# Kernel tuning notes

Hardware: AMD Instinct MI355X
Metric: run time of the kernel (lower is better)

## Reference

```python
import jax, jax.numpy as jnp
import numpy as np

N, P, H, C, E = 50000, 128, 64, 2, 1600000


def setup_inputs() -> dict:
    key = jax.random.key(0)
    ks = jax.random.split(key, 8)
    x = jax.random.normal(ks[0], (N, P), dtype=jnp.float32)
    edge_index = jax.random.randint(ks[1], (2, E), 0, N, dtype=jnp.int32)
    # glorot-ish init for linear weights of the three GCNConv layers
    W1 = jax.random.normal(ks[2], (P, H), dtype=jnp.float32) / np.sqrt(P)
    b1 = jnp.zeros((H,), dtype=jnp.float32)
    W2 = jax.random.normal(ks[3], (H, 2 * H), dtype=jnp.float32) / np.sqrt(H)
    b2 = jnp.zeros((2 * H,), dtype=jnp.float32)
    W3 = jax.random.normal(ks[4], (2 * H, C), dtype=jnp.float32) / np.sqrt(2 * H)
    b3 = jnp.zeros((C,), dtype=jnp.float32)
    return {"x": x, "edge_index": edge_index, "W1": W1, "b1": b1,
            "W2": W2, "b2": b2, "W3": W3, "b3": b3}


def reference(x, edge_index, W1, b1, W2, b2, W3, b3):
    n = x.shape[0]
    # PyG gcn_norm: add self-loops, symmetric D^-1/2 A D^-1/2 normalization
    loops = jnp.arange(n, dtype=edge_index.dtype)
    row = jnp.concatenate([edge_index[0], loops])  # source nodes
    col = jnp.concatenate([edge_index[1], loops])  # target nodes
    deg = jax.ops.segment_sum(jnp.ones_like(row, dtype=x.dtype), col, num_segments=n)
    dinv = jnp.where(deg > 0, jax.lax.rsqrt(deg), 0.0)
    norm = dinv[row] * dinv[col]  # per-edge coefficient [E+N]

    def gcn_conv(h, W, b):
        h = h @ W  # linear transform first (PyG GCNConv order)
        out = jax.ops.segment_sum(norm[:, None] * h[row], col, num_segments=n)
        return out + b

    h = jax.nn.relu(gcn_conv(x, W1, b1))
    # dropout is identity in eval mode
    h = jax.nn.relu(gcn_conv(h, W2, b2))
    h = gcn_conv(h, W3, b3)
    return jax.nn.log_softmax(h, axis=1)
```

## Files before the change

### kernel.cpp

```cpp
#include <hip/hip_runtime.h>
#include <hip/hip_fp16.h>

constexpr int P  = 128;
constexpr int H  = 64;
constexpr int H2 = 128;
constexpr int C  = 2;

constexpr int BW_LOG = 7;
constexpr int BWID   = 128;
constexpr int NBMAX  = 512;
constexpr int T1     = 8192;
constexpr int CAP2   = 15360;

__device__ __forceinline__ unsigned packh2(float a, float b){
  unsigned short la = __half_as_ushort(__float2half_rn(a));
  unsigned short lb = __half_as_ushort(__float2half_rn(b));
  return (unsigned)la | ((unsigned)lb << 16);
}

__global__ void k_zero(int* __restrict__ p, int n){
  int i = blockIdx.x*blockDim.x + threadIdx.x;
  if(i<n) p[i]=0;
}

__global__ __launch_bounds__(256) void k_bhist(const int* __restrict__ col,
                                               int* __restrict__ bcnt, int e, int nb){
  __shared__ int h[NBMAX];
  for(int i=threadIdx.x;i<nb;i+=256) h[i]=0;
  __syncthreads();
  int b0 = blockIdx.x*2048;
  #pragma unroll
  for(int u=0;u<8;u++){
    int idx = b0 + u*256 + threadIdx.x;
    if(idx<e) atomicAdd(&h[col[idx]>>BW_LOG], 1);
  }
  __syncthreads();
  for(int i=threadIdx.x;i<nb;i+=256) if(h[i]) atomicAdd(&bcnt[i], h[i]);
}

__global__ __launch_bounds__(NBMAX) void k_bscan(const int* __restrict__ bcnt,
                                                 int* __restrict__ bstart,
                                                 int* __restrict__ bcursor, int nb){
  __shared__ int sm[NBMAX];
  int t = threadIdx.x;
  int v = (t<nb)? bcnt[t] : 0;
  sm[t]=v; __syncthreads();
  for(int d=1; d<NBMAX; d<<=1){
    int u = (t>=d)? sm[t-d] : 0;
    __syncthreads();
    sm[t]+=u;
    __syncthreads();
  }
  if(t<nb){ int s = sm[t]-v; bstart[t]=s; bcursor[t]=s; }
}

__global__ __launch_bounds__(1024) void k_part(const int* __restrict__ row,
                                               const int* __restrict__ col,
                                               int* __restrict__ bcursor,
                                               unsigned* __restrict__ pairs, int e, int nb){
  __shared__ unsigned stage[T1];
  __shared__ int hist[NBMAX];
  __shared__ int base[NBMAX];
  __shared__ int gpos[NBMAX];
  int tid = threadIdx.x;
  int e0 = blockIdx.x*T1;
  int cnt = min(T1, e-e0);
  for(int i=tid;i<nb;i+=1024) hist[i]=0;
  __syncthreads();
  int myb[8]; int myrank[8]; unsigned mypack[8];
  #pragma unroll
  for(int u=0;u<8;u++){
    int idx = u*1024 + tid;
    if(idx<cnt){
      int c = col[e0+idx], r = row[e0+idx];
      int b = c>>BW_LOG;
      myb[u] = b;
      mypack[u] = ((unsigned)r<<BW_LOG) | (unsigned)(c & (BWID-1));
      myrank[u] = atomicAdd(&hist[b], 1);
    } else myb[u] = -1;
  }
  __syncthreads();
  if(tid<NBMAX) base[tid] = (tid<nb)? hist[tid] : 0;
  __syncthreads();
  for(int d=1; d<NBMAX; d<<=1){
    int u2 = 0;
    if(tid<NBMAX && tid>=d) u2 = base[tid-d];
    __syncthreads();
    if(tid<NBMAX) base[tid] += u2;
    __syncthreads();
  }
  if(tid<nb){
    int ex = base[tid] - hist[tid];
    base[tid] = ex;
    gpos[tid] = atomicAdd(&bcursor[tid], hist[tid]);
  }
  __syncthreads();
  #pragma unroll
  for(int u=0;u<8;u++){
    if(myb[u]>=0) stage[ base[myb[u]] + myrank[u] ] = mypack[u];
  }
  __syncthreads();
  int wave = tid>>6, lane = tid&63;
  for(int b=wave; b<nb; b+=16){
    int len = hist[b], lo = base[b], go = gpos[b];
    for(int k=lane; k<len; k+=64) pairs[go+k] = stage[lo+k];
  }
}

__global__ __launch_bounds__(256) void k_csr(const unsigned* __restrict__ pairs,
                                             const int* __restrict__ bstart,
                                             const int* __restrict__ bcnt,
                                             unsigned* __restrict__ srcA,
                                             int* __restrict__ rowptr,
                                             float* __restrict__ dinv,
                                             int n, int e){
  __shared__ int hist[BWID];
  __shared__ int base[BWID];
  __shared__ int cur[BWID];
  __shared__ unsigned stageS[CAP2];
  int b = blockIdx.x, tid = threadIdx.x;
  int lo = bstart[b], cnt = bcnt[b];
  if(tid<BWID) hist[tid]=0;
  __syncthreads();
  for(int i=tid;i<cnt;i+=256) atomicAdd(&hist[pairs[lo+i] & (BWID-1)], 1);
  __syncthreads();
  if(tid<BWID) base[tid] = hist[tid];
  __syncthreads();
  for(int d=1; d<BWID; d<<=1){
    int u = 0;
    if(tid<BWID && tid>=d) u = base[tid-d];
    __syncthreads();
    if(tid<BWID) base[tid] += u;
    __syncthreads();
  }
  if(tid<BWID){
    int ex = base[tid] - hist[tid];
    base[tid] = ex;
    cur[tid] = ex;
    int node = (b<<BW_LOG) + tid;
    if(node<n){
      rowptr[node] = lo + ex;
      dinv[node]   = rsqrtf((float)hist[tid] + 1.0f);
    }
  }
  if(b==0 && tid==0) rowptr[n] = e;
  __syncthreads();
  if(cnt<=CAP2){
    for(int i=tid;i<cnt;i+=256){
      unsigned p = pairs[lo+i];
      int pos = atomicAdd(&cur[p & (BWID-1)], 1);
      stageS[pos] = p & ~0x7Fu;
    }
    __syncthreads();
    for(int i=tid;i<cnt;i+=256) srcA[lo+i] = stageS[i];
  } else {
    for(int i=tid;i<cnt;i+=256){
      unsigned p = pairs[lo+i];
      int pos = atomicAdd(&cur[p & (BWID-1)], 1);
      srcA[lo+pos] = p & ~0x7Fu;
    }
  }
}

__global__ __launch_bounds__(256) void k_gemm1(const float* __restrict__ x,
                                               const float* __restrict__ W,
                                               const float* __restrict__ dinv,
                                               unsigned* __restrict__ out, int n){
  __shared__ float xs[64][68];
  __shared__ float ws[64][64];
  int tid = threadIdx.x;
  int tx = tid & 15, ty = tid >> 4;
  int r0 = blockIdx.x*64;
  float acc[4][4] = {};
  const float4* x4 = (const float4*)x;
  const float4* W4 = (const float4*)W;
  for(int kh=0; kh<2; ++kh){
    __syncthreads();
    #pragma unroll
    for(int it=0; it<4; ++it){
      int idx = tid + 256*it;
      int r = idx >> 4, k4 = idx & 15;
      int gr = r0 + r;
      float4 v = (gr<n) ? x4[(size_t)gr*32 + kh*16 + k4] : make_float4(0.f,0.f,0.f,0.f);
      *(float4*)&xs[r][4*k4] = v;
    }
    #pragma unroll
    for(int it=0; it<4; ++it){
      int idx = tid + 256*it;
      int kk = idx >> 4, c4 = idx & 15;
      *(float4*)&ws[kk][4*c4] = W4[(size_t)(kh*64+kk)*16 + c4];
    }
    __syncthreads();
    #pragma unroll 8
    for(int kk=0; kk<64; ++kk){
      float xv0 = xs[4*ty+0][kk];
      float xv1 = xs[4*ty+1][kk];
      float xv2 = xs[4*ty+2][kk];
      float xv3 = xs[4*ty+3][kk];
      float4 wv = *(const float4*)&ws[kk][4*tx];
      acc[0][0] += xv0*wv.x; acc[0][1] += xv0*wv.y; acc[0][2] += xv0*wv.z; acc[0][3] += xv0*wv.w;
      acc[1][0] += xv1*wv.x; acc[1][1] += xv1*wv.y; acc[1][2] += xv1*wv.z; acc[1][3] += xv1*wv.w;
      acc[2][0] += xv2*wv.x; acc[2][1] += xv2*wv.y; acc[2][2] += xv2*wv.z; acc[2][3] += xv2*wv.w;
      acc[3][0] += xv3*wv.x; acc[3][1] += xv3*wv.y; acc[3][2] += xv3*wv.z; acc[3][3] += xv3*wv.w;
    }
  }
  #pragma unroll
  for(int i=0;i<4;i++){
    int gr = r0 + 4*ty + i;
    if(gr<n){
      float d = dinv[gr];
      uint2 w;
      w.x = packh2(acc[i][0]*d, acc[i][1]*d);
      w.y = packh2(acc[i][2]*d, acc[i][3]*d);
      *(uint2*)&out[(size_t)gr*32 + 2*tx] = w;
    }
  }
}

__global__ __launch_bounds__(256) void k_gemm23(const float* __restrict__ a2,
                                                const float* __restrict__ W2,
                                                const float* __restrict__ b2,
                                                const float* __restrict__ W3,
                                                const float* __restrict__ dinv,
                                                float* __restrict__ u3, int n){
  __shared__ float as[64][68];
  __shared__ float ws[64][128];
  __shared__ float w3s[H2*C];
  __shared__ float b2s[H2];
  int tid = threadIdx.x;
  int tx = tid & 15, ty = tid >> 4;
  int r0 = blockIdx.x*64;
  const float4* a4 = (const float4*)a2;
  const float4* W24 = (const float4*)W2;
  #pragma unroll
  for(int it=0; it<4; ++it){
    int idx = tid + 256*it;
    int r = idx >> 4, k4 = idx & 15;
    int gr = r0 + r;
    float4 v = (gr<n) ? a4[(size_t)gr*16 + k4] : make_float4(0.f,0.f,0.f,0.f);
    *(float4*)&as[r][4*k4] = v;
  }
  #pragma unroll
  for(int it=0; it<8; ++it){
    int idx = tid + 256*it;
    int kk = idx >> 5, c4 = idx & 31;
    *(float4*)&ws[kk][4*c4] = W24[(size_t)kk*32 + c4];
  }
  if(tid < H2*C) w3s[tid] = W3[tid];
  if(tid < H2)   b2s[tid] = b2[tid];
  __syncthreads();
  float acc[4][8] = {};
  #pragma unroll 4
  for(int kk=0; kk<64; ++kk){
    float xv0 = as[4*ty+0][kk];
    float xv1 = as[4*ty+1][kk];
    float xv2 = as[4*ty+2][kk];
    float xv3 = as[4*ty+3][kk];
    float4 wa = *(const float4*)&ws[kk][8*tx];
    float4 wb = *(const float4*)&ws[kk][8*tx+4];
    acc[0][0]+=xv0*wa.x; acc[0][1]+=xv0*wa.y; acc[0][2]+=xv0*wa.z; acc[0][3]+=xv0*wa.w;
    acc[0][4]+=xv0*wb.x; acc[0][5]+=xv0*wb.y; acc[0][6]+=xv0*wb.z; acc[0][7]+=xv0*wb.w;
    acc[1][0]+=xv1*wa.x; acc[1][1]+=xv1*wa.y; acc[1][2]+=xv1*wa.z; acc[1][3]+=xv1*wa.w;
    acc[1][4]+=xv1*wb.x; acc[1][5]+=xv1*wb.y; acc[1][6]+=xv1*wb.z; acc[1][7]+=xv1*wb.w;
    acc[2][0]+=xv2*wa.x; acc[2][1]+=xv2*wa.y; acc[2][2]+=xv2*wa.z; acc[2][3]+=xv2*wa.w;
    acc[2][4]+=xv2*wb.x; acc[2][5]+=xv2*wb.y; acc[2][6]+=xv2*wb.z; acc[2][7]+=xv2*wb.w;
    acc[3][0]+=xv3*wa.x; acc[3][1]+=xv3*wa.y; acc[3][2]+=xv3*wa.z; acc[3][3]+=xv3*wa.w;
    acc[3][4]+=xv3*wb.x; acc[3][5]+=xv3*wb.y; acc[3][6]+=xv3*wb.z; acc[3][7]+=xv3*wb.w;
  }
  float p[4][2] = {};
  #pragma unroll
  for(int j=0;j<8;j++){
    int c = 8*tx + j;
    float w30 = w3s[2*c], w31 = w3s[2*c+1], bb = b2s[c];
    #pragma unroll
    for(int i=0;i<4;i++){
      float g = fmaxf(acc[i][j] + bb, 0.f);
      p[i][0] += g*w30;
      p[i][1] += g*w31;
    }
  }
  #pragma unroll
  for(int d=1; d<16; d<<=1){
    #pragma unroll
    for(int i=0;i<4;i++){
      p[i][0] += __shfl_xor(p[i][0], d);
      p[i][1] += __shfl_xor(p[i][1], d);
    }
  }
  if(tx==0){
    #pragma unroll
    for(int i=0;i<4;i++){
      int gr = r0 + 4*ty + i;
      if(gr<n){
        float d = dinv[gr];
        u3[2*gr]   = d*p[i][0];
        u3[2*gr+1] = d*p[i][1];
      }
    }
  }
}

template<int MODE>
__global__ __launch_bounds__(256) void k_pullh(const unsigned* __restrict__ src,
                                               const int* __restrict__ rowptr,
                                               const char* __restrict__ tb0,
                                               const float* __restrict__ dinv,
                                               const float* __restrict__ bias,
                                               void* __restrict__ outp, int n){
  int node = blockIdx.x*4 + (threadIdx.x>>6);
  if(node>=n) return;
  int lane = threadIdx.x & 63;
  int slot = lane >> 3;
  int q    = lane & 7;
  const char* tb = tb0 + q*16;
  __half2 h0 = __float2half2_rn(0.f), h1 = h0, h2v = h0, h3 = h0;
  __half2 g0 = h0, g1 = h0, g2v = h0, g3 = h0;
  int beg = rowptr[node], end = rowptr[node+1];
  int j = beg;
  for(; j+16<=end; j+=16){
    unsigned s0 = src[j+slot], s1 = src[j+8+slot];
    uint4 r0 = *(const uint4*)(tb + s0);
    uint4 r1 = *(const uint4*)(tb + s1);
    const __half2* p0 = (const __half2*)&r0;
    const __half2* p1 = (const __half2*)&r1;
    h0 = __hadd2(h0, p0[0]); h1 = __hadd2(h1, p0[1]);
    h2v= __hadd2(h2v,p0[2]); h3 = __hadd2(h3, p0[3]);
    g0 = __hadd2(g0, p1[0]); g1 = __hadd2(g1, p1[1]);
    g2v= __hadd2(g2v,p1[2]); g3 = __hadd2(g3, p1[3]);
  }
  for(; j+8<=end; j+=8){
    unsigned s = src[j+slot];
    uint4 r = *(const uint4*)(tb + s);
    const __half2* p = (const __half2*)&r;
    h0 = __hadd2(h0, p[0]); h1 = __hadd2(h1, p[1]);
    h2v= __hadd2(h2v,p[2]); h3 = __hadd2(h3, p[3]);
  }
  if(j+slot < end){
    unsigned s = src[j+slot];
    uint4 r = *(const uint4*)(tb + s);
    const __half2* p = (const __half2*)&r;
    g0 = __hadd2(g0, p[0]); g1 = __hadd2(g1, p[1]);
    g2v= __hadd2(g2v,p[2]); g3 = __hadd2(g3, p[3]);
  }
  float a[8];
  {
    float2 fa, fb;
    fa = __half22float2(h0); fb = __half22float2(g0); a[0]=fa.x+fb.x; a[1]=fa.y+fb.y;
    fa = __half22float2(h1); fb = __half22float2(g1); a[2]=fa.x+fb.x; a[3]=fa.y+fb.y;
    fa = __half22float2(h2v);fb = __half22float2(g2v);a[4]=fa.x+fb.x; a[5]=fa.y+fb.y;
    fa = __half22float2(h3); fb = __half22float2(g3); a[6]=fa.x+fb.x; a[7]=fa.y+fb.y;
  }
  #pragma unroll
  for(int d=8; d<64; d<<=1){
    #pragma unroll
    for(int i=0;i<8;i++) a[i] += __shfl_xor(a[i], d);
  }
  if(slot==0){
    uint4 sr = *(const uint4*)(tb + (unsigned)node*128u);
    const __half2* p = (const __half2*)&sr;
    float2 f0 = __half22float2(p[0]), f1 = __half22float2(p[1]);
    float2 f2 = __half22float2(p[2]), f3 = __half22float2(p[3]);
    a[0]+=f0.x; a[1]+=f0.y; a[2]+=f1.x; a[3]+=f1.y;
    a[4]+=f2.x; a[5]+=f2.y; a[6]+=f3.x; a[7]+=f3.y;
    float dv = dinv[node];
    if(MODE==1){
      const float* bq = bias + 8*q;
      float o[8];
      #pragma unroll
      for(int i=0;i<8;i++) o[i] = dv * fmaxf(dv*a[i] + bq[i], 0.f);
      uint4 w;
      w.x = packh2(o[0],o[1]); w.y = packh2(o[2],o[3]);
      w.z = packh2(o[4],o[5]); w.w = packh2(o[6],o[7]);
      ((uint4*)outp)[(size_t)node*8 + q] = w;
    } else {
      float* orow = (float*)outp + (size_t)node*64 + 8*q;
      *(float4*)orow     = make_float4(dv*a[0], dv*a[1], dv*a[2], dv*a[3]);
      *(float4*)(orow+4) = make_float4(dv*a[4], dv*a[5], dv*a[6], dv*a[7]);
    }
  }
}

__global__ __launch_bounds__(256) void k_pull2_lsm(const unsigned* __restrict__ src,
                                                   const int* __restrict__ rowptr,
                                                   const float* __restrict__ u3,
                                                   const float* __restrict__ dinv,
                                                   const float* __restrict__ b3,
                                                   float* __restrict__ out, int n){
  int node = blockIdx.x*16 + (threadIdx.x>>4);
  int l16  = threadIdx.x & 15;
  if(node>=n) return;
  const char* ub = (const char*)u3;
  int beg = rowptr[node], end = rowptr[node+1];
  float p0=0.f, p1=0.f, q0=0.f, q1=0.f;
  int j = beg + l16;
  for(; j+16 < end; j += 32){
    float2 A = *(const float2*)(ub + (src[j]    >> 4));
    float2 B = *(const float2*)(ub + (src[j+16] >> 4));
    p0 += A.x; p1 += A.y; q0 += B.x; q1 += B.y;
  }
  if(j < end){
    float2 A = *(const float2*)(ub + (src[j] >> 4));
    p0 += A.x; p1 += A.y;
  }
  p0 += q0; p1 += q1;
  #pragma unroll
  for(int d=1; d<16; d<<=1){ p0 += __shfl_xor(p0,d); p1 += __shfl_xor(p1,d); }
  if(l16==0){
    float d = dinv[node];
    const float2 self = *(const float2*)(ub + (size_t)node*8);
    float z0 = d*(p0 + self.x) + b3[0];
    float z1 = d*(p1 + self.y) + b3[1];
    float m = fmaxf(z0,z1);
    float l = m + logf(expf(z0-m)+expf(z1-m));
    out[2*node]   = z0-l;
    out[2*node+1] = z1-l;
  }
}

extern "C" void kernel_launch(void* const* d_in, const int* in_sizes, int n_in,
                              void* d_out, int out_size, void* d_ws, size_t ws_size,
                              hipStream_t stream){
  const float* x  = (const float*)d_in[0];
  const int*   ei = (const int*)  d_in[1];
  const float* W1 = (const float*)d_in[2];
  const float* b1 = (const float*)d_in[3];
  const float* W2 = (const float*)d_in[4];
  const float* b2 = (const float*)d_in[5];
  const float* W3 = (const float*)d_in[6];
  const float* b3 = (const float*)d_in[7];
  float* out = (float*)d_out;

  const int n = in_sizes[0] / P;
  const int e = in_sizes[1] / 2;
  const int* row = ei;
  const int* col = ei + e;
  const int nb = (n + BWID - 1) >> BW_LOG;

  float* ws   = (float*)d_ws;
  size_t off = 0;
  float* dinv = ws + off; off += n;
  float* R1   = ws + off; off += (size_t)64*n;
  float* R2   = ws + off; off += (size_t)128*n;
  int* rowptr = (int*)(ws + off); off += n+1;
  unsigned* srcA = (unsigned*)(ws + off); off += e;
  int* bcnt   = (int*)(ws + off); off += NBMAX;
  int* bstart = (int*)(ws + off); off += NBMAX;
  int* bcursor= (int*)(ws + off); off += NBMAX;

  unsigned* pairs = (unsigned*)R2;

  unsigned* u1h = (unsigned*)R1;
  unsigned* g1h = (unsigned*)R2;
  float*    a2  = R2 + (size_t)32*n;
  float*    u3  = R1;

  const int BT = 256;

  k_zero <<<(nb+BT-1)/BT, BT, 0, stream>>>(bcnt, nb);
  k_bhist<<<(e+2047)/2048, BT, 0, stream>>>(col, bcnt, e, nb);
  k_bscan<<<1, NBMAX, 0, stream>>>(bcnt, bstart, bcursor, nb);
  k_part <<<(e+T1-1)/T1, 1024, 0, stream>>>(row, col, bcursor, pairs, e, nb);
  k_csr  <<<nb, BT, 0, stream>>>(pairs, bstart, bcnt, srcA, rowptr, dinv, n, e);

  k_gemm1<<<(n+63)/64, BT, 0, stream>>>(x, W1, dinv, u1h, n);

  const int pg = (n+3)/4;
  k_pullh<1><<<pg, BT, 0, stream>>>(srcA, rowptr, (const char*)u1h, dinv, b1, (void*)g1h, n);
  k_pullh<2><<<pg, BT, 0, stream>>>(srcA, rowptr, (const char*)g1h, dinv, nullptr, (void*)a2, n);

  k_gemm23<<<(n+63)/64, BT, 0, stream>>>(a2, W2, b2, W3, dinv, u3, n);
  k_pull2_lsm<<<(n+15)/16, BT, 0, stream>>>(srcA, rowptr, u3, dinv, b3, out, n);
}
```

Before: 180.3 us.

## Store layer-2 aggregate in fp16, use wave-shuffle scans, unroll gather loop

The second aggregation pass now writes fp16 instead of fp32, and the fused layer-2/3 GEMM reads and converts it. This halves that intermediate's write and read traffic at some precision cost. The block-level shared-memory prefix scans in the partition and CSR kernels are replaced by single-wave register and shuffle scans, which cuts many barriers. The half-precision gather loop gains a 32-edge unrolled stage for more loads in flight, and the zeroing kernel becomes a memset. Buffers are rearranged so u3 sits after the fp16 a2 in R1.

Measured after the change: 179.1 us. Within noise of the previous version (-0.6%).

```diff
diff --git a/kernel.cpp b/kernel.cpp
--- a/kernel.cpp
+++ b/kernel.cpp
@@ -16,11 +16,6 @@
   unsigned short la = __half_as_ushort(__float2half_rn(a));
   unsigned short lb = __half_as_ushort(__float2half_rn(b));
   return (unsigned)la | ((unsigned)lb << 16);
-}
-
-__global__ void k_zero(int* __restrict__ p, int n){
-  int i = blockIdx.x*blockDim.x + threadIdx.x;
-  if(i<n) p[i]=0;
 }
 
 __global__ __launch_bounds__(256) void k_bhist(const int* __restrict__ col,
@@ -65,7 +60,7 @@
   int tid = threadIdx.x;
   int e0 = blockIdx.x*T1;
   int cnt = min(T1, e-e0);
-  for(int i=tid;i<nb;i+=1024) hist[i]=0;
+  for(int i=tid;i<NBMAX;i+=1024) hist[i]=0;
   __syncthreads();
   int myb[8]; int myrank[8]; unsigned mypack[8];
   #pragma unroll
@@ -80,20 +75,21 @@
     } else myb[u] = -1;
   }
   __syncthreads();
-  if(tid<NBMAX) base[tid] = (tid<nb)? hist[tid] : 0;
-  __syncthreads();
-  for(int d=1; d<NBMAX; d<<=1){
-    int u2 = 0;
-    if(tid<NBMAX && tid>=d) u2 = base[tid-d];
-    __syncthreads();
-    if(tid<NBMAX) base[tid] += u2;
-    __syncthreads();
-  }
-  if(tid<nb){
-    int ex = base[tid] - hist[tid];
-    base[tid] = ex;
-    gpos[tid] = atomicAdd(&bcursor[tid], hist[tid]);
-  }
+  if(tid<64){
+    int v[8]; int sum=0;
+    #pragma unroll
+    for(int i=0;i<8;i++) v[i]=hist[tid*8+i];
+    #pragma unroll
+    for(int i=0;i<8;i++){ int t=v[i]; v[i]=sum; sum+=t; }
+    int run=sum;
+    #pragma unroll
+    for(int d=1; d<64; d<<=1){ int u=__shfl_up(run,d); if(tid>=d) run+=u; }
+    int excl = run - sum;
+    #pragma unroll
+    for(int i=0;i<8;i++) base[tid*8+i] = excl + v[i];
+  }
+  __syncthreads();
+  if(tid<nb) gpos[tid] = atomicAdd(&bcursor[tid], hist[tid]);
   __syncthreads();
   #pragma unroll
   for(int u=0;u<8;u++){
@@ -124,18 +120,19 @@
   __syncthreads();
   for(int i=tid;i<cnt;i+=256) atomicAdd(&hist[pairs[lo+i] & (BWID-1)], 1);
   __syncthreads();
-  if(tid<BWID) base[tid] = hist[tid];
-  __syncthreads();
-  for(int d=1; d<BWID; d<<=1){
-    int u = 0;
-    if(tid<BWID && tid>=d) u = base[tid-d];
-    __syncthreads();
-    if(tid<BWID) base[tid] += u;
-    __syncthreads();
-  }
+  if(tid<64){
+    int v0=hist[2*tid], v1=hist[2*tid+1];
+    int sum=v0+v1;
+    int run=sum;
+    #pragma unroll
+    for(int d=1; d<64; d<<=1){ int u=__shfl_up(run,d); if(tid>=d) run+=u; }
+    int excl = run - sum;
+    base[2*tid]   = excl;
+    base[2*tid+1] = excl + v0;
+  }
+  __syncthreads();
   if(tid<BWID){
-    int ex = base[tid] - hist[tid];
-    base[tid] = ex;
+    int ex = base[tid];
     cur[tid] = ex;
     int node = (b<<BW_LOG) + tid;
     if(node<n){
@@ -217,7 +214,7 @@
   }
 }
 
-__global__ __launch_bounds__(256) void k_gemm23(const float* __restrict__ a2,
+__global__ __launch_bounds__(256) void k_gemm23(const unsigned* __restrict__ a2h,
                                                 const float* __restrict__ W2,
                                                 const float* __restrict__ b2,
                                                 const float* __restrict__ W3,
@@ -230,15 +227,20 @@
   int tid = threadIdx.x;
   int tx = tid & 15, ty = tid >> 4;
   int r0 = blockIdx.x*64;
-  const float4* a4 = (const float4*)a2;
+  const uint4* a16 = (const uint4*)a2h;
   const float4* W24 = (const float4*)W2;
   #pragma unroll
-  for(int it=0; it<4; ++it){
+  for(int it=0; it<2; ++it){
     int idx = tid + 256*it;
-    int r = idx >> 4, k4 = idx & 15;
+    int r = idx >> 3, u = idx & 7;
     int gr = r0 + r;
-    float4 v = (gr<n) ? a4[(size_t)gr*16 + k4] : make_float4(0.f,0.f,0.f,0.f);
-    *(float4*)&as[r][4*k4] = v;
+    uint4 v = (gr<n) ? a16[(size_t)gr*8 + u] : make_uint4(0,0,0,0);
+    const __half2* hp = (const __half2*)&v;
+    float2 f0=__half22float2(hp[0]), f1=__half22float2(hp[1]);
+    float2 f2=__half22float2(hp[2]), f3=__half22float2(hp[3]);
+    float* dst = &as[r][8*u];
+    dst[0]=f0.x; dst[1]=f0.y; dst[2]=f1.x; dst[3]=f1.y;
+    dst[4]=f2.x; dst[5]=f2.y; dst[6]=f3.x; dst[7]=f3.y;
   }
   #pragma unroll
   for(int it=0; it<8; ++it){
@@ -306,7 +308,7 @@
                                                const char* __restrict__ tb0,
                                                const float* __restrict__ dinv,
                                                const float* __restrict__ bias,
-                                               void* __restrict__ outp, int n){
+                                               unsigned* __restrict__ outp, int n){
   int node = blockIdx.x*4 + (threadIdx.x>>6);
   if(node>=n) return;
   int lane = threadIdx.x & 63;
@@ -317,6 +319,26 @@
   __half2 g0 = h0, g1 = h0, g2v = h0, g3 = h0;
   int beg = rowptr[node], end = rowptr[node+1];
   int j = beg;
+  for(; j+32<=end; j+=32){
+    unsigned s0 = src[j+slot],    s1 = src[j+8+slot];
+    unsigned s2 = src[j+16+slot], s3 = src[j+24+slot];
+    uint4 r0 = *(const uint4*)(tb + s0);
+    uint4 r1 = *(const uint4*)(tb + s1);
+    uint4 r2 = *(const uint4*)(tb + s2);
+    uint4 r3 = *(const uint4*)(tb + s3);
+    const __half2* p0 = (const __half2*)&r0;
+    const __half2* p1 = (const __half2*)&r1;
+    const __half2* p2 = (const __half2*)&r2;
+    const __half2* p3 = (const __half2*)&r3;
+    h0 = __hadd2(h0, p0[0]); h1 = __hadd2(h1, p0[1]);
+    h2v= __hadd2(h2v,p0[2]); h3 = __hadd2(h3, p0[3]);
+    g0 = __hadd2(g0, p1[0]); g1 = __hadd2(g1, p1[1]);
+    g2v= __hadd2(g2v,p1[2]); g3 = __hadd2(g3, p1[3]);
+    h0 = __hadd2(h0, p2[0]); h1 = __hadd2(h1, p2[1]);
+    h2v= __hadd2(h2v,p2[2]); h3 = __hadd2(h3, p2[3]);
+    g0 = __hadd2(g0, p3[0]); g1 = __hadd2(g1, p3[1]);
+    g2v= __hadd2(g2v,p3[2]); g3 = __hadd2(g3, p3[3]);
+  }
   for(; j+16<=end; j+=16){
     unsigned s0 = src[j+slot], s1 = src[j+8+slot];
     uint4 r0 = *(const uint4*)(tb + s0);
@@ -363,20 +385,19 @@
     a[0]+=f0.x; a[1]+=f0.y; a[2]+=f1.x; a[3]+=f1.y;
     a[4]+=f2.x; a[5]+=f2.y; a[6]+=f3.x; a[7]+=f3.y;
     float dv = dinv[node];
+    uint4 w;
     if(MODE==1){
       const float* bq = bias + 8*q;
       float o[8];
       #pragma unroll
       for(int i=0;i<8;i++) o[i] = dv * fmaxf(dv*a[i] + bq[i], 0.f);
-      uint4 w;
       w.x = packh2(o[0],o[1]); w.y = packh2(o[2],o[3]);
       w.z = packh2(o[4],o[5]); w.w = packh2(o[6],o[7]);
-      ((uint4*)outp)[(size_t)node*8 + q] = w;
     } else {
-      float* orow = (float*)outp + (size_t)node*64 + 8*q;
-      *(float4*)orow     = make_float4(dv*a[0], dv*a[1], dv*a[2], dv*a[3]);
-      *(float4*)(orow+4) = make_float4(dv*a[4], dv*a[5], dv*a[6], dv*a[7]);
-    }
+      w.x = packh2(dv*a[0], dv*a[1]); w.y = packh2(dv*a[2], dv*a[3]);
+      w.z = packh2(dv*a[4], dv*a[5]); w.w = packh2(dv*a[6], dv*a[7]);
+    }
+    ((uint4*)outp)[(size_t)node*8 + q] = w;
   }
 }
 
@@ -451,12 +472,12 @@
 
   unsigned* u1h = (unsigned*)R1;
   unsigned* g1h = (unsigned*)R2;
-  float*    a2  = R2 + (size_t)32*n;
-  float*    u3  = R1;
+  unsigned* a2h = (unsigned*)R1;
+  float*    u3  = R1 + (size_t)32*n;
 
   const int BT = 256;
 
-  k_zero <<<(nb+BT-1)/BT, BT, 0, stream>>>(bcnt, nb);
+  hipMemsetAsync(bcnt, 0, NBMAX*sizeof(int), stream);
   k_bhist<<<(e+2047)/2048, BT, 0, stream>>>(col, bcnt, e, nb);
   k_bscan<<<1, NBMAX, 0, stream>>>(bcnt, bstart, bcursor, nb);
   k_part <<<(e+T1-1)/T1, 1024, 0, stream>>>(row, col, bcursor, pairs, e, nb);
@@ -465,9 +486,9 @@
   k_gemm1<<<(n+63)/64, BT, 0, stream>>>(x, W1, dinv, u1h, n);
 
   const int pg = (n+3)/4;
-  k_pullh<1><<<pg, BT, 0, stream>>>(srcA, rowptr, (const char*)u1h, dinv, b1, (void*)g1h, n);
-  k_pullh<2><<<pg, BT, 0, stream>>>(srcA, rowptr, (const char*)g1h, dinv, nullptr, (void*)a2, n);
-
-  k_gemm23<<<(n+63)/64, BT, 0, stream>>>(a2, W2, b2, W3, dinv, u3, n);
+  k_pullh<1><<<pg, BT, 0, stream>>>(srcA, rowptr, (const char*)u1h, dinv, b1, g1h, n);
+  k_pullh<2><<<pg, BT, 0, stream>>>(srcA, rowptr, (const char*)g1h, dinv, nullptr, a2h, n);
+
+  k_gemm23<<<(n+63)/64, BT, 0, stream>>>(a2h, W2, b2, W3, dinv, u3, n);
   k_pull2_lsm<<<(n+15)/16, BT, 0, stream>>>(srcA, rowptr, u3, dinv, b3, out, n);
 }
```
